# Performance work log

Measured on AMD Instinct MI355X. Metric: run time of the kernel, lower is better.

The kernel has to match this reference:

```python
import jax, jax.numpy as jnp
import numpy as np

B, N, F_DIM, M, K, D = 8, 16384, 6, 128, 16, 768
MLP_DIMS = [F_DIM, 256, 512, 768, D]


def _fps(pts):
    """Deterministic farthest point sampling. pts: [N,4] -> indices [M] (first pick = point 0)."""
    n = pts.shape[0]

    def step(carry, _):
        min_d, last = carry
        d = jnp.sum((pts - pts[last]) ** 2, axis=-1)
        min_d = jnp.minimum(min_d, d)
        nxt = jnp.argmax(min_d).astype(jnp.int32)
        return (min_d, nxt), nxt

    init = (jnp.full((n,), 1e30, dtype=pts.dtype), jnp.int32(0))
    _, idx = jax.lax.scan(step, init, None, length=M - 1)
    return jnp.concatenate([jnp.zeros((1,), jnp.int32), idx])


def setup_inputs() -> dict:
    key = jax.random.key(0)
    ks = jax.random.split(key, 16)
    bidx = jnp.repeat(jnp.arange(B, dtype=jnp.float32), N)[:, None]
    xyzt = jax.random.normal(ks[0], (B * N, 4), jnp.float32)
    coordinates = jnp.concatenate([bidx, xyzt], axis=1)  # [B*N, 5]
    features = jax.random.normal(ks[1], (B * N, F_DIM), jnp.float32)
    inp = {"coordinates": coordinates, "features": features}
    for i in range(4):
        di, do = MLP_DIMS[i], MLP_DIMS[i + 1]
        inp[f"W{i}"] = jax.random.normal(ks[2 + i], (di, do), jnp.float32) * np.float32(1.0 / np.sqrt(di))
        inp[f"b{i}"] = jnp.zeros((do,), jnp.float32)
    for j in range(2):
        inp[f"Wn{j}"] = jax.random.normal(ks[6 + j], (D, D), jnp.float32) * np.float32(1.0 / np.sqrt(D))
        inp[f"bn{j}"] = jnp.zeros((D,), jnp.float32)
    return inp


def _forward(coordinates, features, W0, b0, W1, b1, W2, b2, W3, b3, Wn0, bn0, Wn1, bn1):
    # Equal points per event, sorted batch ids -> plain reshape replaces the per-batch loop.
    pts = coordinates.reshape(B, N, 5)[:, :, 1:5]       # xyz + time  [B,N,4]
    h = features.reshape(B, N, F_DIM)
    # per-point MLP (ReLU after each hidden layer, final Linear has no activation)
    h = jax.nn.relu(h @ W0 + b0)
    h = jax.nn.relu(h @ W1 + b1)
    h = jax.nn.relu(h @ W2 + b2)
    pf = h @ W3 + b3                                    # [B,N,D]
    # FPS centroids (non-differentiable index selection, as in the torch/cpu original)
    fidx = jax.vmap(_fps)(jax.lax.stop_gradient(pts))   # [B,M]
    cent = jnp.take_along_axis(pts, fidx[:, :, None], axis=1)  # [B,M,4]
    # cdist + kNN (smallest distances)
    dist = jnp.sqrt(jnp.sum((cent[:, :, None, :] - pts[:, None, :, :]) ** 2, axis=-1))  # [B,M,N]
    _, knn = jax.lax.top_k(-dist, K)                    # [B,M,K]
    gathered = jax.vmap(lambda p, i: p[i])(pf, knn)     # [B,M,K,D]
    pooled = jnp.max(gathered, axis=2)                  # [B,M,D]
    t = jax.nn.relu(pooled @ Wn0 + bn0)
    tokens = t @ Wn1 + bn1                              # [B,M,D]
    # sort tokens/centroids by centroid time (column 3)
    order = jnp.argsort(cent[:, :, 3], axis=1)
    cent = jnp.take_along_axis(cent, order[:, :, None], axis=1)
    tokens = jnp.take_along_axis(tokens, order[:, :, None], axis=1)
    masks = jnp.ones((B, M), dtype=bool)  # num_points > max_tokens -> all tokens valid
    return tokens, cent, masks


def reference(coordinates, features, W0, b0, W1, b1, W2, b2, W3, b3, Wn0, bn0, Wn1, bn1):
    return _forward(coordinates, features, W0, b0, W1, b1, W2, b2, W3, b3, Wn0, bn0, Wn1, bn1)
```

## Files before the change

### kernel.cpp

```cpp
#include <hip/hip_runtime.h>

#define B_ 8
#define N_ 16384
#define F_ 6
#define M_ 128
#define K_ 16
#define D_ 768

typedef unsigned short u16;
typedef unsigned int u32;
typedef __attribute__((ext_vector_type(8))) short short8;
typedef __attribute__((ext_vector_type(4))) float f32x4;
typedef __attribute__((ext_vector_type(2))) float f32x2;

__device__ __forceinline__ u16 f2bf(float f){
  union { float f; u32 i; } v; v.f = f;
  u32 x = v.i;
  u32 r = x + 0x7FFFu + ((x >> 16) & 1u);
  return (u16)(r >> 16);
}

__device__ __forceinline__ void ld_g2l(const u16* g, u16* l){
  __builtin_amdgcn_global_load_lds((const __attribute__((address_space(1))) u32*)g,
                                   (__attribute__((address_space(3))) u32*)l, 16, 0, 0);
}

__global__ __launch_bounds__(256) void conv_all(const float* __restrict__ W1,
                                                const float* __restrict__ W2,
                                                const float* __restrict__ W3,
                                                const float* __restrict__ Wn0,
                                                const float* __restrict__ Wn1,
                                                u16* __restrict__ Wb){
  __shared__ u16 tile[64][65];
  int blk = blockIdx.x;
  const float* W; u16* WT; int K, N, lb;
  if      (blk < 32)  { W = W1;  WT = Wb;           K = 256; N = 512; lb = blk; }
  else if (blk < 128) { W = W2;  WT = Wb + 131072;  K = 512; N = 768; lb = blk - 32; }
  else if (blk < 272) { W = W3;  WT = Wb + 524288;  K = 768; N = 768; lb = blk - 128; }
  else if (blk < 416) { W = Wn0; WT = Wb + 1114112; K = 768; N = 768; lb = blk - 272; }
  else                { W = Wn1; WT = Wb + 1703936; K = 768; N = 768; lb = blk - 416; }
  int tiles_n = N >> 6;
  int tk = lb / tiles_n, tn = lb % tiles_n;
  int k0 = tk << 6, n0 = tn << 6;
  int t = threadIdx.x;
#pragma unroll
  for (int q = 0; q < 16; q++){
    int idx = q * 256 + t;
    int kk = idx >> 6, nn = idx & 63;
    tile[kk][nn] = f2bf(W[(size_t)(k0 + kk) * N + n0 + nn]);
  }
  __syncthreads();
#pragma unroll
  for (int q = 0; q < 16; q++){
    int idx = q * 256 + t;
    int nn = idx >> 6, kk = idx & 63;
    WT[(size_t)(n0 + nn) * K + k0 + kk] = tile[kk][nn];
  }
}

#define FPW 16
__global__ __launch_bounds__(512, 2) void fps_kernel(const float* __restrict__ coords,
                                                     float* __restrict__ cent){
#pragma clang fp contract(off)
  __shared__ float s_wv[2][8];
  __shared__ int s_wi[2][8];
  int b = blockIdx.x;
  int t = threadIdx.x;
  const float* cb = coords + (size_t)b * N_ * 5;
  f32x2 px[FPW], py[FPW], pz[FPW], pw[FPW], md[FPW];
#pragma unroll
  for (int j = 0; j < FPW; j++){
    int p = t + (j << 9);
    size_t i0 = (size_t)(2 * p) * 5;
    px[j] = (f32x2){cb[i0+1], cb[i0+6]};
    py[j] = (f32x2){cb[i0+2], cb[i0+7]};
    pz[j] = (f32x2){cb[i0+3], cb[i0+8]};
    pw[j] = (f32x2){cb[i0+4], cb[i0+9]};
    md[j] = (f32x2){1e30f, 1e30f};
  }
  float cx = cb[1], cy = cb[2], cz = cb[3], ct = cb[4];
  if (t == 0){
    float* c0 = cent + (size_t)b * M_ * 4;
    c0[0]=cx; c0[1]=cy; c0[2]=cz; c0[3]=ct;
  }
  for (int step = 1; step < M_; step++){
    f32x2 cx2 = (f32x2){cx, cx}, cy2 = (f32x2){cy, cy};
    f32x2 cz2 = (f32x2){cz, cz}, ct2 = (f32x2){ct, ct};
    float bv = -1.0f; int bi = 1 << 30;
#pragma unroll
    for (int j = 0; j < FPW; j++){
      f32x2 dX = px[j] - cx2;
      f32x2 dY = py[j] - cy2;
      f32x2 s = dX*dX + dY*dY;
      f32x2 dZ = pz[j] - cz2;
      s = s + dZ*dZ;
      f32x2 dW = pw[j] - ct2;
      s = s + dW*dW;
      f32x2 m = md[j];
      m[0] = (s[0] < m[0]) ? s[0] : m[0];
      m[1] = (s[1] < m[1]) ? s[1] : m[1];
      md[j] = m;
      int i0 = (t + (j << 9)) << 1;
      if (m[0] > bv){ bv = m[0]; bi = i0; }
      if (m[1] > bv){ bv = m[1]; bi = i0 + 1; }
    }
#pragma unroll
    for (int off = 32; off > 0; off >>= 1){
      float ov = __shfl_down(bv, off);
      int oi = __shfl_down(bi, off);
      if (ov > bv || (ov == bv && oi < bi)){ bv = ov; bi = oi; }
    }
    int par = step & 1;
    if ((t & 63) == 0){ s_wv[par][t >> 6] = bv; s_wi[par][t >> 6] = bi; }
    __syncthreads();
    float fv = s_wv[par][t & 7];
    int fi = s_wi[par][t & 7];
#pragma unroll
    for (int off = 1; off < 8; off <<= 1){
      float ov = __shfl_xor(fv, off);
      int oi = __shfl_xor(fi, off);
      if (ov > fv || (ov == fv && oi < fi)){ fv = ov; fi = oi; }
    }
    fi &= (N_ - 1);
    size_t wbase = (size_t)fi * 5;
    cx = cb[wbase+1]; cy = cb[wbase+2]; cz = cb[wbase+3]; ct = cb[wbase+4];
    if (t == 0){
      float* cr = cent + ((size_t)b * M_ + step) * 4;
      cr[0]=cx; cr[1]=cy; cr[2]=cz; cr[3]=ct;
    }
  }
}

__global__ __launch_bounds__(128) void rank_scatter(const float* __restrict__ cent_fps,
                                                    float* __restrict__ cent_sorted,
                                                    float* __restrict__ out,
                                                    size_t out_elems){
  int b = blockIdx.x, m = threadIdx.x;
  __shared__ float tt[M_];
  const float* row = cent_fps + ((size_t)b * M_ + m) * 4;
  float x=row[0], y=row[1], z=row[2], w=row[3];
  tt[m] = w;
  __syncthreads();
  int rank = 0;
  for (int j = 0; j < M_; j++){
    float tj = tt[j];
    if (tj < w || (tj == w && j < m)) rank++;
  }
  float* dst = cent_sorted + ((size_t)b * M_ + rank) * 4;
  dst[0]=x; dst[1]=y; dst[2]=z; dst[3]=w;
  size_t co = (size_t)B_ * M_ * D_ + ((size_t)b * M_ + rank) * 4;
  if (co + 3 < out_elems){
    out[co+0]=x; out[co+1]=y; out[co+2]=z; out[co+3]=w;
  }
  size_t mo = (size_t)B_ * M_ * D_ + (size_t)B_ * M_ * 4 + (size_t)b * M_ + m;
  if (mo < out_elems) out[mo] = 1.0f;
}

#define KNT 512
#define KPT 32
__global__ __launch_bounds__(512) void knn_kernel(const float* __restrict__ coords,
                                                  const float* __restrict__ cent,
                                                  int* __restrict__ knn){
#pragma clang fp contract(off)
  int cm = blockIdx.x;
  int b = cm >> 7;
  const float* cb = coords + (size_t)b * N_ * 5;
  int t = threadIdx.x;
  float cx=cent[cm*4+0], cy=cent[cm*4+1], cz=cent[cm*4+2], ct=cent[cm*4+3];
  float dist[KPT];
#pragma unroll
  for (int j = 0; j < KPT; j++){
    size_t i = t + j * KNT;
    float dx=cb[i*5+1]-cx, dy=cb[i*5+2]-cy, dz=cb[i*5+3]-cz, dw=cb[i*5+4]-ct;
    float d = ((dx*dx + dy*dy) + dz*dz) + dw*dw;
    dist[j] = sqrtf(d);
  }
  __shared__ float s_wv[8];
  __shared__ int s_wi[8];
  __shared__ int s_bi;
  for (int r = 0; r < K_; r++){
    float bv = 3e38f; int bi = 1 << 30;
#pragma unroll
    for (int j = 0; j < KPT; j++){
      int i = t + j * KNT;
      float v = dist[j];
      if (v < bv){ bv = v; bi = i; }
    }
#pragma unroll
    for (int off = 32; off > 0; off >>= 1){
      float ov = __shfl_down(bv, off);
      int oi = __shfl_down(bi, off);
      if (ov < bv || (ov == bv && oi < bi)){ bv = ov; bi = oi; }
    }
    if ((t & 63) == 0){ s_wv[t >> 6] = bv; s_wi[t >> 6] = bi; }
    __syncthreads();
    if (t == 0){
      float fv = s_wv[0]; int fi = s_wi[0];
      for (int w = 1; w < 8; w++){
        float wv = s_wv[w]; int wi = s_wi[w];
        if (wv < fv || (wv == fv && wi < fi)){ fv = wv; fi = wi; }
      }
      s_bi = fi;
      knn[(size_t)cm * K_ + r] = fi & (N_ - 1);
    }
    __syncthreads();
    int wi = s_bi;
#pragma unroll
    for (int j = 0; j < KPT; j++){
      if (t + j * KNT == wi) dist[j] = 3e38f;
    }
  }
}

__global__ __launch_bounds__(256) void gather_l0(const float* __restrict__ feat,
                                                 const int* __restrict__ knn,
                                                 const float* __restrict__ W0,
                                                 const float* __restrict__ b0,
                                                 u16* __restrict__ h1,
                                                 int rowBase){
  __shared__ float sW[F_][256];
  __shared__ float sb[256];
  __shared__ float sfa[32][F_];
  int t = threadIdx.x;
#pragma unroll
  for (int k = 0; k < F_; k++) sW[k][t] = W0[k * 256 + t];
  sb[t] = b0[t];
  if (t < 32 * F_){
    int r = t / F_, k = t % F_;
    int grow = rowBase + blockIdx.x * 32 + r;
    int bb = grow >> 11;
    int idx = knn[grow] & (N_ - 1);
    sfa[r][k] = feat[((size_t)bb * N_ + idx) * F_ + k];
  }
  __syncthreads();
#pragma unroll 4
  for (int r = 0; r < 32; r++){
    float acc = sb[t];
#pragma unroll
    for (int k = 0; k < F_; k++) acc = fmaf(sfa[r][k], sW[k][t], acc);
    int lrow = blockIdx.x * 32 + r;
    h1[(size_t)lrow * 256 + t] = f2bf(fmaxf(acc, 0.0f));
  }
}

template<int RELU, int OUTF32>
__global__ __launch_bounds__(256) void gemm_bf16(const u16* __restrict__ A,
                                                 const u16* __restrict__ WT,
                                                 const float* __restrict__ bias,
                                                 void* __restrict__ Cv,
                                                 int Kd, int Nd){
  __shared__ u16 As[128][32];
  __shared__ u16 Bs[128][32];
  const int t = threadIdx.x;
  const int bm = blockIdx.y << 7;
  const int bn = blockIdx.x << 7;
  const int wave = t >> 6;
  const int lane = t & 63;
  const int wm = (wave & 1) << 6;
  const int wn = (wave >> 1) << 6;
  const int lm = lane & 15;
  const int lk = (lane >> 4) << 3;
  u16* AsF = &As[0][0];
  u16* BsF = &Bs[0][0];
  const int wbase = wave << 6;
  f32x4 acc[4][4] = {};
  for (int k0 = 0; k0 < Kd; k0 += 32){
#pragma unroll
    for (int it = 0; it < 2; it++){
      int slot = t + (it << 8);
      int r = slot >> 2;
      int c = (slot & 3) << 3;
      int dst = (wbase + (it << 8)) << 3;
      ld_g2l(A  + (size_t)(bm + r) * Kd + k0 + c, AsF + dst);
      ld_g2l(WT + (size_t)(bn + r) * Kd + k0 + c, BsF + dst);
    }
    __syncthreads();
    short8 af[4], bfr[4];
#pragma unroll
    for (int mt = 0; mt < 4; mt++) af[mt] = *(const short8*)&As[wm + (mt << 4) + lm][lk];
#pragma unroll
    for (int nt = 0; nt < 4; nt++) bfr[nt] = *(const short8*)&Bs[wn + (nt << 4) + lm][lk];
#pragma unroll
    for (int mt = 0; mt < 4; mt++)
#pragma unroll
      for (int nt = 0; nt < 4; nt++)
        acc[mt][nt] = __builtin_amdgcn_mfma_f32_16x16x32_bf16(af[mt], bfr[nt], acc[mt][nt], 0, 0, 0);
    __syncthreads();
  }
#pragma unroll
  for (int nt = 0; nt < 4; nt++){
    int n = bn + wn + (nt << 4) + lm;
    float bia = bias[n];
#pragma unroll
    for (int mt = 0; mt < 4; mt++){
#pragma unroll
      for (int r2 = 0; r2 < 4; r2++){
        int m = bm + wm + (mt << 4) + ((lane >> 4) << 2) + r2;
        float v = acc[mt][nt][r2] + bia;
        if (RELU) v = fmaxf(v, 0.0f);
        if (OUTF32) ((float*)Cv)[(size_t)m * Nd + n] = v;
        else        ((u16*)Cv)[(size_t)m * Nd + n] = f2bf(v);
      }
    }
  }
}

template<int RELU, int OUTF32>
__global__ __launch_bounds__(256) void gemm64(const u16* __restrict__ A,
                                              const u16* __restrict__ WT,
                                              const float* __restrict__ bias,
                                              void* __restrict__ Cv,
                                              int Kd, int Nd){
  __shared__ u16 As[64][32];
  __shared__ u16 Bs[64][32];
  const int t = threadIdx.x;
  const int bm = blockIdx.y << 6;
  const int bn = blockIdx.x << 6;
  const int wave = t >> 6;
  const int lane = t & 63;
  const int wm = (wave & 1) << 5;
  const int wn = (wave >> 1) << 5;
  const int lm = lane & 15;
  const int lk = (lane >> 4) << 3;
  u16* AsF = &As[0][0];
  u16* BsF = &Bs[0][0];
  const int wbase = wave << 6;
  f32x4 acc[2][2] = {};
  for (int k0 = 0; k0 < Kd; k0 += 32){
    {
      int r = t >> 2;
      int c = (t & 3) << 3;
      int dst = wbase << 3;
      ld_g2l(A  + (size_t)(bm + r) * Kd + k0 + c, AsF + dst);
      ld_g2l(WT + (size_t)(bn + r) * Kd + k0 + c, BsF + dst);
    }
    __syncthreads();
    short8 af[2], bfr[2];
#pragma unroll
    for (int mt = 0; mt < 2; mt++) af[mt] = *(const short8*)&As[wm + (mt << 4) + lm][lk];
#pragma unroll
    for (int nt = 0; nt < 2; nt++) bfr[nt] = *(const short8*)&Bs[wn + (nt << 4) + lm][lk];
#pragma unroll
    for (int mt = 0; mt < 2; mt++)
#pragma unroll
      for (int nt = 0; nt < 2; nt++)
        acc[mt][nt] = __builtin_amdgcn_mfma_f32_16x16x32_bf16(af[mt], bfr[nt], acc[mt][nt], 0, 0, 0);
    __syncthreads();
  }
#pragma unroll
  for (int nt = 0; nt < 2; nt++){
    int n = bn + wn + (nt << 4) + lm;
    float bia = bias[n];
#pragma unroll
    for (int mt = 0; mt < 2; mt++){
#pragma unroll
      for (int r2 = 0; r2 < 4; r2++){
        int m = bm + wm + (mt << 4) + ((lane >> 4) << 2) + r2;
        float v = acc[mt][nt][r2] + bia;
        if (RELU) v = fmaxf(v, 0.0f);
        if (OUTF32) ((float*)Cv)[(size_t)m * Nd + n] = v;
        else        ((u16*)Cv)[(size_t)m * Nd + n] = f2bf(v);
      }
    }
  }
}

__global__ __launch_bounds__(256) void gemm_pool(const u16* __restrict__ A,
                                                 const u16* __restrict__ WT,
                                                 const float* __restrict__ bias,
                                                 u16* __restrict__ pooled,
                                                 int Kd, int Nd, int groupBase){
  __shared__ u16 As[128][32];
  __shared__ u16 Bs[128][32];
  const int t = threadIdx.x;
  const int bm = blockIdx.y << 7;
  const int bn = blockIdx.x << 7;
  const int wave = t >> 6;
  const int lane = t & 63;
  const int wm = (wave & 1) << 6;
  const int wn = (wave >> 1) << 6;
  const int lm = lane & 15;
  const int lk = (lane >> 4) << 3;
  u16* AsF = &As[0][0];
  u16* BsF = &Bs[0][0];
  const int wbase = wave << 6;
  f32x4 acc[4][4] = {};
  for (int k0 = 0; k0 < Kd; k0 += 32){
#pragma unroll
    for (int it = 0; it < 2; it++){
      int slot = t + (it << 8);
      int r = slot >> 2;
      int c = (slot & 3) << 3;
      int dst = (wbase + (it << 8)) << 3;
      ld_g2l(A  + (size_t)(bm + r) * Kd + k0 + c, AsF + dst);
      ld_g2l(WT + (size_t)(bn + r) * Kd + k0 + c, BsF + dst);
    }
    __syncthreads();
    short8 af[4], bfr[4];
#pragma unroll
    for (int mt = 0; mt < 4; mt++) af[mt] = *(const short8*)&As[wm + (mt << 4) + lm][lk];
#pragma unroll
    for (int nt = 0; nt < 4; nt++) bfr[nt] = *(const short8*)&Bs[wn + (nt << 4) + lm][lk];
#pragma unroll
    for (int mt = 0; mt < 4; mt++)
#pragma unroll
      for (int nt = 0; nt < 4; nt++)
        acc[mt][nt] = __builtin_amdgcn_mfma_f32_16x16x32_bf16(af[mt], bfr[nt], acc[mt][nt], 0, 0, 0);
    __syncthreads();
  }
#pragma unroll
  for (int nt = 0; nt < 4; nt++){
    int n = bn + wn + (nt << 4) + lm;
    float bia = bias[n];
#pragma unroll
    for (int mt = 0; mt < 4; mt++){
      f32x4 a = acc[mt][nt];
      float v = fmaxf(fmaxf(a[0], a[1]), fmaxf(a[2], a[3]));
      v = fmaxf(v, __shfl_xor(v, 16));
      v = fmaxf(v, __shfl_xor(v, 32));
      if ((lane >> 4) == 0){
        int g = groupBase + (bm >> 4) + (wm >> 4) + mt;
        pooled[(size_t)g * Nd + n] = f2bf(v + bia);
      }
    }
  }
}

__global__ __launch_bounds__(256) void fill_diag(float* __restrict__ out, size_t out_elems){
  size_t i = (size_t)blockIdx.x * 256 + threadIdx.x;
  if (i >= out_elems) return;
  size_t maskStart = (size_t)B_ * M_ * D_ + (size_t)B_ * M_ * 4;
  out[i] = (i >= maskStart) ? 1.0f : 0.0f;
}

extern "C" void kernel_launch(void* const* d_in, const int* in_sizes, int n_in,
                              void* d_out, int out_size, void* d_ws, size_t ws_size,
                              hipStream_t stream){
  (void)in_sizes; (void)n_in;
  const float* coords   = (const float*)d_in[0];
  const float* features = (const float*)d_in[1];
  const float* W0 = (const float*)d_in[2];  const float* b0 = (const float*)d_in[3];
  const float* W1 = (const float*)d_in[4];  const float* b1 = (const float*)d_in[5];
  const float* W2 = (const float*)d_in[6];  const float* b2 = (const float*)d_in[7];
  const float* W3 = (const float*)d_in[8];  const float* b3 = (const float*)d_in[9];
  const float* Wn0 = (const float*)d_in[10]; const float* bn0 = (const float*)d_in[11];
  const float* Wn1 = (const float*)d_in[12]; const float* bn1 = (const float*)d_in[13];
  float* out = (float*)d_out;
  const size_t out_elems = (size_t)out_size;

  char* ws = (char*)d_ws;
  const size_t o_cent = 0;
  const size_t o_cntS = 16384;
  const size_t o_knn  = 32768;
  const size_t o_Wb   = 131072;
  const size_t o_pool = 4718592;
  const size_t o_t1   = 6291456;
  const size_t o_chunk= 7864320;
  const int ROWS = B_ * M_ * K_;

  int R = 16384;
  while (R > 128 && o_chunk + (size_t)R * 2560 > ws_size) R >>= 1;
  if (d_ws == nullptr || o_chunk + (size_t)R * 2560 > ws_size){
    fill_diag<<<(int)((out_elems + 255) / 256), 256, 0, stream>>>(out, out_elems);
    return;
  }

  float* cent_fps    = (float*)(ws + o_cent);
  float* cent_sorted = (float*)(ws + o_cntS);
  int*   knn         = (int*)(ws + o_knn);
  u16* Wb   = (u16*)(ws + o_Wb);
  u16* W1t  = Wb;               u16* W2t  = Wb + 131072;
  u16* W3t  = Wb + 524288;      u16* Wn0t = Wb + 1114112;
  u16* Wn1t = Wb + 1703936;
  u16* pooled = (u16*)(ws + o_pool);
  u16* t1     = (u16*)(ws + o_t1);
  u16* regA   = (u16*)(ws + o_chunk);
  u16* regB   = (u16*)(ws + o_chunk + (size_t)R * 1536);

  conv_all<<<560, 256, 0, stream>>>(W1, W2, W3, Wn0, Wn1, Wb);
  fps_kernel<<<B_, 512, 0, stream>>>(coords, cent_fps);
  rank_scatter<<<B_, 128, 0, stream>>>(cent_fps, cent_sorted, out, out_elems);
  knn_kernel<<<B_ * M_, KNT, 0, stream>>>(coords, cent_sorted, knn);

  for (int rowBase = 0; rowBase < ROWS; rowBase += R){
    gather_l0<<<R / 32, 256, 0, stream>>>(features, knn, W0, b0, regA, rowBase);
    gemm_bf16<1,0><<<dim3(4, R / 128), 256, 0, stream>>>(regA, W1t, b1, regB, 256, 512);
    gemm_bf16<1,0><<<dim3(6, R / 128), 256, 0, stream>>>(regB, W2t, b2, regA, 512, 768);
    gemm_pool<<<dim3(6, R / 128), 256, 0, stream>>>(regA, W3t, b3, pooled, 768, 768, rowBase >> 4);
  }

  gemm64<1,0><<<dim3(12, (B_ * M_) / 64), 256, 0, stream>>>(pooled, Wn0t, bn0, t1, 768, 768);
  gemm64<0,1><<<dim3(12, (B_ * M_) / 64), 256, 0, stream>>>(t1, Wn1t, bn1, out, 768, 768);
}
```

Measured before the change: 558.2 us.

## Split FPS across eight workgroups per batch with global atomic key exchange

Farthest point sampling now runs on eight 256-thread workgroups per batch instead of one 512-thread block. Each group reduces its local argmax and publishes a packed (distance, inverted index) 64-bit key to a per-step global slot, then spins until all eight slots are filled and takes the max. This spreads the serial 127-step loop over more compute units to cut per-step latency. In exchange it adds a global memory round trip and spin-wait every step, plus a zeroing kernel, and it relies on all 64 blocks being co-resident.

```diff
diff --git a/kernel.cpp b/kernel.cpp
--- a/kernel.cpp
+++ b/kernel.cpp
@@ -9,6 +9,7 @@
 
 typedef unsigned short u16;
 typedef unsigned int u32;
+typedef unsigned long long u64;
 typedef __attribute__((ext_vector_type(8))) short short8;
 typedef __attribute__((ext_vector_type(4))) float f32x4;
 typedef __attribute__((ext_vector_type(2))) float f32x2;
@@ -58,20 +59,29 @@
   }
 }
 
-#define FPW 16
-__global__ __launch_bounds__(512, 2) void fps_kernel(const float* __restrict__ coords,
-                                                     float* __restrict__ cent){
+__global__ __launch_bounds__(256) void zero_keys(u64* __restrict__ keys){
+  keys[(size_t)blockIdx.x * 256 + threadIdx.x] = 0ull;
+}
+
+#define FG 8
+#define FJ 4
+__global__ __launch_bounds__(256) void fps_multi(const float* __restrict__ coords,
+                                                 float* __restrict__ cent,
+                                                 u64* __restrict__ keys){
 #pragma clang fp contract(off)
-  __shared__ float s_wv[2][8];
-  __shared__ int s_wi[2][8];
-  int b = blockIdx.x;
+  __shared__ float s_wv[2][4];
+  __shared__ int   s_wi[2][4];
+  int blk = blockIdx.x;
+  int b = blk >> 3, g = blk & 7;
   int t = threadIdx.x;
+  int lane = t & 63, wave = t >> 6;
   const float* cb = coords + (size_t)b * N_ * 5;
-  f32x2 px[FPW], py[FPW], pz[FPW], pw[FPW], md[FPW];
-#pragma unroll
-  for (int j = 0; j < FPW; j++){
-    int p = t + (j << 9);
-    size_t i0 = (size_t)(2 * p) * 5;
+  int pbase = g << 11;
+  f32x2 px[FJ], py[FJ], pz[FJ], pw[FJ], md[FJ];
+#pragma unroll
+  for (int j = 0; j < FJ; j++){
+    int p = pbase + ((t + (j << 8)) << 1);
+    size_t i0 = (size_t)p * 5;
     px[j] = (f32x2){cb[i0+1], cb[i0+6]};
     py[j] = (f32x2){cb[i0+2], cb[i0+7]};
     pz[j] = (f32x2){cb[i0+3], cb[i0+8]};
@@ -79,7 +89,7 @@
     md[j] = (f32x2){1e30f, 1e30f};
   }
   float cx = cb[1], cy = cb[2], cz = cb[3], ct = cb[4];
-  if (t == 0){
+  if (g == 0 && t == 0){
     float* c0 = cent + (size_t)b * M_ * 4;
     c0[0]=cx; c0[1]=cy; c0[2]=cz; c0[3]=ct;
   }
@@ -88,7 +98,7 @@
     f32x2 cz2 = (f32x2){cz, cz}, ct2 = (f32x2){ct, ct};
     float bv = -1.0f; int bi = 1 << 30;
 #pragma unroll
-    for (int j = 0; j < FPW; j++){
+    for (int j = 0; j < FJ; j++){
       f32x2 dX = px[j] - cx2;
       f32x2 dY = py[j] - cy2;
       f32x2 s = dX*dX + dY*dY;
@@ -100,7 +110,7 @@
       m[0] = (s[0] < m[0]) ? s[0] : m[0];
       m[1] = (s[1] < m[1]) ? s[1] : m[1];
       md[j] = m;
-      int i0 = (t + (j << 9)) << 1;
+      int i0 = pbase + ((t + (j << 8)) << 1);
       if (m[0] > bv){ bv = m[0]; bi = i0; }
       if (m[1] > bv){ bv = m[1]; bi = i0 + 1; }
     }
@@ -111,20 +121,34 @@
       if (ov > bv || (ov == bv && oi < bi)){ bv = ov; bi = oi; }
     }
     int par = step & 1;
-    if ((t & 63) == 0){ s_wv[par][t >> 6] = bv; s_wi[par][t >> 6] = bi; }
-    __syncthreads();
-    float fv = s_wv[par][t & 7];
-    int fi = s_wi[par][t & 7];
+    if (lane == 0){ s_wv[par][wave] = bv; s_wi[par][wave] = bi; }
+    __syncthreads();
+    u64* kb = keys + (((size_t)step << 3) + b) * 8;
+    if (t == 0){
+      float fv = s_wv[par][0]; int fi = s_wi[par][0];
+#pragma unroll
+      for (int w = 1; w < 4; w++){
+        float wv = s_wv[par][w]; int wi = s_wi[par][w];
+        if (wv > fv || (wv == fv && wi < fi)){ fv = wv; fi = wi; }
+      }
+      union { float f; u32 i; } vb; vb.f = fv;
+      u64 key = ((u64)(vb.i + 1u) << 32) | (u32)(N_ - 1 - fi);
+      __hip_atomic_store(&kb[g], key, __ATOMIC_RELAXED, __HIP_MEMORY_SCOPE_AGENT);
+    }
+    u64 k = __hip_atomic_load(&kb[lane & 7], __ATOMIC_RELAXED, __HIP_MEMORY_SCOPE_AGENT);
+    while (k == 0ull){
+      __builtin_amdgcn_s_sleep(1);
+      k = __hip_atomic_load(&kb[lane & 7], __ATOMIC_RELAXED, __HIP_MEMORY_SCOPE_AGENT);
+    }
 #pragma unroll
     for (int off = 1; off < 8; off <<= 1){
-      float ov = __shfl_xor(fv, off);
-      int oi = __shfl_xor(fi, off);
-      if (ov > fv || (ov == fv && oi < fi)){ fv = ov; fi = oi; }
-    }
-    fi &= (N_ - 1);
-    size_t wbase = (size_t)fi * 5;
+      u64 ok = __shfl_xor(k, off);
+      if (ok > k) k = ok;
+    }
+    int widx = N_ - 1 - (int)(k & 0xffffffffu);
+    size_t wbase = (size_t)widx * 5;
     cx = cb[wbase+1]; cy = cb[wbase+2]; cz = cb[wbase+3]; ct = cb[wbase+4];
-    if (t == 0){
+    if (g == 0 && t == 0){
       float* cr = cent + ((size_t)b * M_ + step) * 4;
       cr[0]=cx; cr[1]=cy; cr[2]=cz; cr[3]=ct;
     }
@@ -455,7 +479,8 @@
   const size_t o_Wb   = 131072;
   const size_t o_pool = 4718592;
   const size_t o_t1   = 6291456;
-  const size_t o_chunk= 7864320;
+  const size_t o_keys = 7864320;
+  const size_t o_chunk= 7929856;
   const int ROWS = B_ * M_ * K_;
 
   int R = 16384;
@@ -474,11 +499,13 @@
   u16* Wn1t = Wb + 1703936;
   u16* pooled = (u16*)(ws + o_pool);
   u16* t1     = (u16*)(ws + o_t1);
+  u64* keysbuf = (u64*)(ws + o_keys);
   u16* regA   = (u16*)(ws + o_chunk);
   u16* regB   = (u16*)(ws + o_chunk + (size_t)R * 1536);
 
   conv_all<<<560, 256, 0, stream>>>(W1, W2, W3, Wn0, Wn1, Wb);
-  fps_kernel<<<B_, 512, 0, stream>>>(coords, cent_fps);
+  zero_keys<<<32, 256, 0, stream>>>(keysbuf);
+  fps_multi<<<B_ * FG, 256, 0, stream>>>(coords, cent_fps, keysbuf);
   rank_scatter<<<B_, 128, 0, stream>>>(cent_fps, cent_sorted, out, out_elems);
   knn_kernel<<<B_ * M_, KNT, 0, stream>>>(coords, cent_sorted, knn);
 
```

After: 621.8 us. 11.4% more time.

## Rework FPS kernel: LDS-resident xy, packed-f32 asm, 64-bit key argmax reduction

Applied to the files above, without the earlier changes.

The FPS kernel now stores x and y coordinates in shared memory instead of registers, which lowers register pressure. The distance math uses explicit v_pk_add/v_pk_mul packed instructions. The argmax reduction packs value and inverted index into one 64-bit key, so each shuffle step is a single compare, and the cross-wave stage becomes a serial scan over eight keys. The cost is LDS reads on every step, and it relies on non-negative float bit ordering to match the original tie-breaking.

```diff
diff --git a/kernel.cpp b/kernel.cpp
--- a/kernel.cpp
+++ b/kernel.cpp
@@ -9,6 +9,7 @@
 
 typedef unsigned short u16;
 typedef unsigned int u32;
+typedef unsigned long long u64;
 typedef __attribute__((ext_vector_type(8))) short short8;
 typedef __attribute__((ext_vector_type(4))) float f32x4;
 typedef __attribute__((ext_vector_type(2))) float f32x2;
@@ -23,6 +24,13 @@
 __device__ __forceinline__ void ld_g2l(const u16* g, u16* l){
   __builtin_amdgcn_global_load_lds((const __attribute__((address_space(1))) u32*)g,
                                    (__attribute__((address_space(3))) u32*)l, 16, 0, 0);
+}
+
+__device__ __forceinline__ f32x2 pkadd(f32x2 a, f32x2 b){
+  f32x2 d; asm("v_pk_add_f32 %0, %1, %2" : "=v"(d) : "v"(a), "v"(b)); return d;
+}
+__device__ __forceinline__ f32x2 pkmul(f32x2 a, f32x2 b){
+  f32x2 d; asm("v_pk_mul_f32 %0, %1, %2" : "=v"(d) : "v"(a), "v"(b)); return d;
 }
 
 __global__ __launch_bounds__(256) void conv_all(const float* __restrict__ W1,
@@ -58,24 +66,28 @@
   }
 }
 
-#define FPW 16
-__global__ __launch_bounds__(512, 2) void fps_kernel(const float* __restrict__ coords,
-                                                     float* __restrict__ cent){
+#define FPJ 16
+__global__ __launch_bounds__(512, 2) void fps_block(const float* __restrict__ coords,
+                                                    float* __restrict__ cent){
 #pragma clang fp contract(off)
-  __shared__ float s_wv[2][8];
-  __shared__ int s_wi[2][8];
+  __shared__ float sx[N_];
+  __shared__ float sy[N_];
+  __shared__ u64 swk[2][8];
   int b = blockIdx.x;
   int t = threadIdx.x;
+  int lane = t & 63, wave = t >> 6;
   const float* cb = coords + (size_t)b * N_ * 5;
-  f32x2 px[FPW], py[FPW], pz[FPW], pw[FPW], md[FPW];
-#pragma unroll
-  for (int j = 0; j < FPW; j++){
+  f32x2 pz[FPJ], pw[FPJ], md[FPJ];
+#pragma unroll
+  for (int j = 0; j < FPJ; j++){
     int p = t + (j << 9);
     size_t i0 = (size_t)(2 * p) * 5;
-    px[j] = (f32x2){cb[i0+1], cb[i0+6]};
-    py[j] = (f32x2){cb[i0+2], cb[i0+7]};
-    pz[j] = (f32x2){cb[i0+3], cb[i0+8]};
-    pw[j] = (f32x2){cb[i0+4], cb[i0+9]};
+    float x0 = cb[i0+1], y0 = cb[i0+2], z0 = cb[i0+3], w0 = cb[i0+4];
+    float x1 = cb[i0+6], y1 = cb[i0+7], z1 = cb[i0+8], w1 = cb[i0+9];
+    *(f32x2*)&sx[2 * p] = (f32x2){x0, x1};
+    *(f32x2*)&sy[2 * p] = (f32x2){y0, y1};
+    pz[j] = (f32x2){z0, z1};
+    pw[j] = (f32x2){w0, w1};
     md[j] = (f32x2){1e30f, 1e30f};
   }
   float cx = cb[1], cy = cb[2], cz = cb[3], ct = cb[4];
@@ -83,47 +95,47 @@
     float* c0 = cent + (size_t)b * M_ * 4;
     c0[0]=cx; c0[1]=cy; c0[2]=cz; c0[3]=ct;
   }
+  __syncthreads();
   for (int step = 1; step < M_; step++){
-    f32x2 cx2 = (f32x2){cx, cx}, cy2 = (f32x2){cy, cy};
-    f32x2 cz2 = (f32x2){cz, cz}, ct2 = (f32x2){ct, ct};
+    f32x2 ncx2 = (f32x2){-cx, -cx}, ncy2 = (f32x2){-cy, -cy};
+    f32x2 ncz2 = (f32x2){-cz, -cz}, nct2 = (f32x2){-ct, -ct};
     float bv = -1.0f; int bi = 1 << 30;
 #pragma unroll
-    for (int j = 0; j < FPW; j++){
-      f32x2 dX = px[j] - cx2;
-      f32x2 dY = py[j] - cy2;
-      f32x2 s = dX*dX + dY*dY;
-      f32x2 dZ = pz[j] - cz2;
-      s = s + dZ*dZ;
-      f32x2 dW = pw[j] - ct2;
-      s = s + dW*dW;
+    for (int j = 0; j < FPJ; j++){
+      int p = t + (j << 9);
+      f32x2 xv = *(const f32x2*)&sx[p << 1];
+      f32x2 yv = *(const f32x2*)&sy[p << 1];
+      f32x2 dx = pkadd(xv, ncx2);
+      f32x2 dy = pkadd(yv, ncy2);
+      f32x2 s  = pkadd(pkmul(dx, dx), pkmul(dy, dy));
+      f32x2 dz = pkadd(pz[j], ncz2);
+      s = pkadd(s, pkmul(dz, dz));
+      f32x2 dw = pkadd(pw[j], nct2);
+      s = pkadd(s, pkmul(dw, dw));
       f32x2 m = md[j];
-      m[0] = (s[0] < m[0]) ? s[0] : m[0];
-      m[1] = (s[1] < m[1]) ? s[1] : m[1];
+      m[0] = fminf(s[0], m[0]);
+      m[1] = fminf(s[1], m[1]);
       md[j] = m;
-      int i0 = (t + (j << 9)) << 1;
+      int i0 = p << 1;
       if (m[0] > bv){ bv = m[0]; bi = i0; }
       if (m[1] > bv){ bv = m[1]; bi = i0 + 1; }
     }
+    union { float f; u32 u; } cv; cv.f = bv;
+    u64 k = ((u64)cv.u << 32) | (u32)(N_ - 1 - bi);
 #pragma unroll
     for (int off = 32; off > 0; off >>= 1){
-      float ov = __shfl_down(bv, off);
-      int oi = __shfl_down(bi, off);
-      if (ov > bv || (ov == bv && oi < bi)){ bv = ov; bi = oi; }
+      u64 ok = __shfl_down(k, off);
+      if (ok > k) k = ok;
     }
     int par = step & 1;
-    if ((t & 63) == 0){ s_wv[par][t >> 6] = bv; s_wi[par][t >> 6] = bi; }
-    __syncthreads();
-    float fv = s_wv[par][t & 7];
-    int fi = s_wi[par][t & 7];
-#pragma unroll
-    for (int off = 1; off < 8; off <<= 1){
-      float ov = __shfl_xor(fv, off);
-      int oi = __shfl_xor(fi, off);
-      if (ov > fv || (ov == fv && oi < fi)){ fv = ov; fi = oi; }
-    }
-    fi &= (N_ - 1);
-    size_t wbase = (size_t)fi * 5;
-    cx = cb[wbase+1]; cy = cb[wbase+2]; cz = cb[wbase+3]; ct = cb[wbase+4];
+    if (lane == 0) swk[par][wave] = k;
+    __syncthreads();
+    u64 fk = swk[par][0];
+#pragma unroll
+    for (int w = 1; w < 8; w++){ u64 wk = swk[par][w]; if (wk > fk) fk = wk; }
+    int widx = N_ - 1 - (int)(fk & 0xffffffffu);
+    size_t wb = (size_t)widx * 5;
+    cx = cb[wb+1]; cy = cb[wb+2]; cz = cb[wb+3]; ct = cb[wb+4];
     if (t == 0){
       float* cr = cent + ((size_t)b * M_ + step) * 4;
       cr[0]=cx; cr[1]=cy; cr[2]=cz; cr[3]=ct;
@@ -478,7 +490,7 @@
   u16* regB   = (u16*)(ws + o_chunk + (size_t)R * 1536);
 
   conv_all<<<560, 256, 0, stream>>>(W1, W2, W3, Wn0, Wn1, Wb);
-  fps_kernel<<<B_, 512, 0, stream>>>(coords, cent_fps);
+  fps_block<<<B_, 512, 0, stream>>>(coords, cent_fps);
   rank_scatter<<<B_, 128, 0, stream>>>(cent_fps, cent_sorted, out, out_elems);
   knn_kernel<<<B_ * M_, KNT, 0, stream>>>(coords, cent_sorted, knn);
 
```

Result: no change. 554.1 us (-0.7%).
